# Kernel optimization log

Measured on AMD Instinct MI355X. Metric: run time of the kernel, lower is better.

The kernel has to match this reference:

```python
import jax, jax.numpy as jnp
import numpy as np
import math

HEAD_NUM = 16


def setup_inputs() -> dict:
    key = jax.random.key(0)
    ks = jax.random.split(key, 6)
    B, S, E = 2, 2048, 1024
    sc = 1.0 / math.sqrt(E)
    return {
        "x": jax.random.normal(ks[0], (B, S, E), dtype=jnp.float32),
        "mask": jnp.ones((B, S), dtype=jnp.int32),
        "Wq": jax.random.normal(ks[1], (E, E), dtype=jnp.float32) * sc,
        "bq": jnp.zeros((E,), dtype=jnp.float32),
        "Wk": jax.random.normal(ks[2], (E, E), dtype=jnp.float32) * sc,
        "bk": jnp.zeros((E,), dtype=jnp.float32),
        "Wv": jax.random.normal(ks[3], (E, E), dtype=jnp.float32) * sc,
        "bv": jnp.zeros((E,), dtype=jnp.float32),
        "Wo": jax.random.normal(ks[4], (E, E), dtype=jnp.float32) * sc,
        "bo": jnp.zeros((E,), dtype=jnp.float32),
    }


def reference(x, mask, Wq, bq, Wk, bk, Wv, bv, Wo, bo):
    B, S, E = x.shape
    H = HEAD_NUM
    D = E // H
    # Projections (nn.Linear: x @ W^T + b; W here stored so that x @ W is equivalent)
    q = (x @ Wq + bq).reshape(B, S, H, D).transpose(0, 2, 1, 3)  # [B,H,S,D]
    k = (x @ Wk + bk).reshape(B, S, H, D).transpose(0, 2, 1, 3)
    v = (x @ Wv + bv).reshape(B, S, H, D).transpose(0, 2, 1, 3)
    score = jnp.einsum("bhqd,bhkd->bhqk", q, k) / jnp.sqrt(jnp.asarray(D, x.dtype))
    # Faithful to source: masked positions (mask==0) are filled with +inf
    m = mask[:, None, None, :]  # [B,1,1,S]
    score = jnp.where(m == 0, jnp.inf, score)
    attn = jax.nn.softmax(score, axis=-1)
    # dropout is identity in eval mode
    out = jnp.einsum("bhqk,bhkd->bhqd", attn, v)
    out = out.transpose(0, 2, 1, 3).reshape(B, S, E)
    return out @ Wo + bo
```

## Files before the change

### kernel.cpp

```cpp
#include <hip/hip_runtime.h>
#include <hip/hip_bf16.h>
#include <math.h>


#define S_LEN 2048
#define EMB   1024
#define HN    16
#define HD    64
#define BATCH 2
#define MROWS (BATCH * S_LEN)
#define NEL   ((size_t)MROWS * EMB)

typedef _Float16 f16x8 __attribute__((ext_vector_type(8)));
typedef _Float16 f16x4 __attribute__((ext_vector_type(4)));
typedef _Float16 f16x2 __attribute__((ext_vector_type(2)));
typedef float    f32x4  __attribute__((ext_vector_type(4)));
typedef float    f32x16 __attribute__((ext_vector_type(16)));
typedef unsigned u32x4  __attribute__((ext_vector_type(4)));

#define GLOAD_LDS16(g, l) \
  __builtin_amdgcn_global_load_lds((const __attribute__((address_space(1))) void*)(g), \
                                   (__attribute__((address_space(3))) void*)(l), 16, 0, 0)

__device__ __forceinline__ float exp2fast(float x) {
#if __has_builtin(__builtin_amdgcn_exp2f)
  return __builtin_amdgcn_exp2f(x);
#else
  return __expf(x * 0.69314718056f);
#endif
}

__device__ __forceinline__ unsigned pk_f16(float a, float b) {
#if __has_builtin(__builtin_amdgcn_cvt_pkrtz)
  auto h = __builtin_amdgcn_cvt_pkrtz(a, b);
  return __builtin_bit_cast(unsigned, h);
#else
  unsigned lo = (unsigned)__builtin_bit_cast(unsigned short, (_Float16)a);
  unsigned hi = (unsigned)__builtin_bit_cast(unsigned short, (_Float16)b);
  return lo | (hi << 16);
#endif
}

__device__ __forceinline__ float dot2acc(unsigned p, float acc) {
#if __has_builtin(__builtin_amdgcn_fdot2)
  f16x2 ones = {(_Float16)1.0f, (_Float16)1.0f};
  return __builtin_amdgcn_fdot2(__builtin_bit_cast(f16x2, p), ones, acc, false);
#else
  f16x2 v = __builtin_bit_cast(f16x2, p);
  return acc + (float)v[0] + (float)v[1];
#endif
}

__device__ __forceinline__ f32x16 mfma32(f16x8 a, f16x8 b, f32x16 c) {
  return __builtin_amdgcn_mfma_f32_32x32x16_f16(a, b, c, 0, 0, 0);
}
__device__ __forceinline__ f32x4 mfma16(f16x8 a, f16x8 b, f32x4 c) {
  return __builtin_amdgcn_mfma_f32_16x16x32_f16(a, b, c, 0, 0, 0);
}

__global__ __launch_bounds__(256)
void prep_f16(const float* __restrict__ x,
              const float* __restrict__ Wq, const float* __restrict__ Wk,
              const float* __restrict__ Wv, const float* __restrict__ Wo,
              _Float16* __restrict__ xf, _Float16* __restrict__ Wt,
              _Float16* __restrict__ Wot) {
  __shared__ float tile[64][65];
  const int bid = blockIdx.x;
  const int tt  = threadIdx.x;
  if (bid < 2048) {
    const int i = bid * 256 + tt;
    const float4* s = (const float4*)x + (size_t)i * 2;
    float4 a = s[0], b = s[1];
    f16x8 o = {(_Float16)a.x, (_Float16)a.y, (_Float16)a.z, (_Float16)a.w,
               (_Float16)b.x, (_Float16)b.y, (_Float16)b.z, (_Float16)b.w};
    *((f16x8*)xf + i) = o;
    return;
  }
  const int j   = bid - 2048;
  const int job = j >> 8;
  const int tl  = j & 255;
  const int bn  = (tl & 15) * 64, bk = (tl >> 4) * 64;
  const float* W = (job == 0) ? Wq : (job == 1) ? Wk : (job == 2) ? Wv : Wo;
  _Float16* dst = (job == 3) ? Wot : Wt + (size_t)job * EMB * EMB;
  const int c = tt & 63, r4 = tt >> 6;
#pragma unroll
  for (int jj = 0; jj < 16; ++jj) {
    int r = r4 * 16 + jj;
    tile[r][c] = W[(size_t)(bk + r) * EMB + bn + c];
  }
  __syncthreads();
#pragma unroll
  for (int jj = 0; jj < 16; ++jj) {
    int rr = r4 * 16 + jj;
    dst[(size_t)(bn + rr) * EMB + bk + c] = (_Float16)tile[c][rr];
  }
}

template<bool SW>
__device__ __forceinline__ void gemm_kloop(
    const _Float16* __restrict__ gA, const _Float16* __restrict__ gB,
    _Float16* As, _Float16* Bs, int w,
    int wr, int wc, int ln, int kg, f32x4 (&acc)[4][4]) {
  const int dst = w * 1024;
#define GSTAGE(buf, k0) do { \
    GLOAD_LDS16(gA + (k0),            As + (buf) * 4096 + dst); \
    GLOAD_LDS16(gA + (k0) + 16 * EMB, As + (buf) * 4096 + dst + 512); \
    GLOAD_LDS16(gB + (k0),            Bs + (buf) * 4096 + dst); \
    GLOAD_LDS16(gB + (k0) + 16 * EMB, Bs + (buf) * 4096 + dst + 512); \
  } while (0)
  GSTAGE(0, 0);
  int cur = 0;
#pragma unroll 1
  for (int k0 = 0; k0 < EMB; k0 += 32) {
    __syncthreads();
    if (k0 + 32 < EMB) GSTAGE(cur ^ 1, k0 + 32);
    const _Float16* Ab = As + cur * 4096;
    const _Float16* Bb = Bs + cur * 4096;
    f16x8 a[4], b[4];
#pragma unroll
    for (int mi = 0; mi < 4; ++mi)
      a[mi] = *(const f16x8*)&Ab[(wr * 64 + mi * 16 + ln) * 32 + kg * 8];
#pragma unroll
    for (int ni = 0; ni < 4; ++ni)
      b[ni] = *(const f16x8*)&Bb[(wc * 64 + ni * 16 + ln) * 32 + kg * 8];
#pragma unroll
    for (int mi = 0; mi < 4; ++mi)
#pragma unroll
      for (int ni = 0; ni < 4; ++ni)
        acc[mi][ni] = SW ? mfma16(b[ni], a[mi], acc[mi][ni])
                         : mfma16(a[mi], b[ni], acc[mi][ni]);
    cur ^= 1;
  }
#undef GSTAGE
}

template<int MODE>
__global__ __launch_bounds__(256)
void gemm_f16(const _Float16* __restrict__ A, const _Float16* __restrict__ Bt,
              int Ncols,
              _Float16* __restrict__ qf, _Float16* __restrict__ kf,
              _Float16* __restrict__ vf, float* __restrict__ outF,
              const float* __restrict__ b0, const float* __restrict__ b1,
              const float* __restrict__ b2) {
  __shared__ _Float16 As[2 * 128 * 32];
  __shared__ _Float16 Bs[2 * 128 * 32];
  const int tid  = threadIdx.x;
  const int lane = tid & 63, w = tid >> 6;
  const int ln = lane & 15, kg = lane >> 4;
  const int wr = w >> 1, wc = w & 1;

  const int nbx  = Ncols >> 7;
  const int ncpx = nbx >> 3;
  const int xcd  = blockIdx.x & 7;
  const int idx  = blockIdx.x >> 3;
  const int col0 = (xcd * ncpx + idx % ncpx) << 7;
  const int row0 = (idx / ncpx) << 7;

  const int cA0 = w * 128 + lane;
  const int arow0 = cA0 >> 2, acol0 = (cA0 & 3) * 8;

  f32x4 acc[4][4];
#pragma unroll
  for (int mi = 0; mi < 4; ++mi)
#pragma unroll
    for (int ni = 0; ni < 4; ++ni) acc[mi][ni] = (f32x4){0.f, 0.f, 0.f, 0.f};

  const _Float16* gA = A  + (size_t)(row0 + arow0) * EMB + acol0;
  const _Float16* gB = Bt + (size_t)(col0 + arow0) * EMB + acol0;

  const bool is_v = (MODE == 0) && (col0 >= 2048);
  if (is_v) gemm_kloop<true >(gA, gB, As, Bs, w, wr, wc, ln, kg, acc);
  else      gemm_kloop<false>(gA, gB, As, Bs, w, wr, wc, ln, kg, acc);

  if (MODE == 1) {
#pragma unroll
    for (int mi = 0; mi < 4; ++mi)
#pragma unroll
      for (int ni = 0; ni < 4; ++ni) {
        const int n = col0 + wc * 64 + ni * 16 + ln;
        const float bias = b0[n];
#pragma unroll
        for (int r = 0; r < 4; ++r) {
          const int m = row0 + wr * 64 + mi * 16 + kg * 4 + r;
          outF[(size_t)m * EMB + n] = acc[mi][ni][r] + bias;
        }
      }
  } else if (!is_v) {
#pragma unroll
    for (int mi = 0; mi < 4; ++mi)
#pragma unroll
      for (int ni = 0; ni < 4; ++ni) {
        const int n = col0 + wc * 64 + ni * 16 + ln;
        const int mat = n >> 10, e = n & 1023;
        const float bias = (mat == 0 ? b0 : b1)[e];
        const int h = e >> 6, d = e & 63;
#pragma unroll
        for (int r = 0; r < 4; ++r) {
          const int m = row0 + wr * 64 + mi * 16 + kg * 4 + r;
          const int bb = m >> 11, ss = m & 2047;
          const int bh = bb * HN + h;
          float val = acc[mi][ni][r] + bias;
          if (mat == 0) {
            qf[((size_t)bh * S_LEN + ss) * HD + d] = (_Float16)(val * 0.18033688f);
          } else {
            kf[((size_t)bh * S_LEN + ss) * HD + d] = (_Float16)val;
          }
        }
      }
  } else {
#pragma unroll
    for (int mi = 0; mi < 4; ++mi)
#pragma unroll
      for (int ni = 0; ni < 4; ++ni) {
#pragma unroll
        for (int r = 0; r < 4; ++r) {
          const int n = col0 + wc * 64 + ni * 16 + kg * 4 + r;
          const int e = n - 2048;
          const int h = e >> 6, d = e & 63;
          const int m = row0 + wr * 64 + mi * 16 + ln;
          const int bb = m >> 11, ss = m & 2047;
          const int ssp = (ss & ~12) | ((ss & 4) << 1) | ((ss & 8) >> 1);
          const int bh = bb * HN + h;
          float val = acc[mi][ni][r] + b2[e];
          vf[((size_t)bh * HD + d) * S_LEN + ssp] = (_Float16)val;
        }
      }
  }
}

__global__ __launch_bounds__(512)
void attn_f16v5(const _Float16* __restrict__ Qf, const _Float16* __restrict__ Kf,
                const _Float16* __restrict__ VfT, _Float16* __restrict__ Of) {
  __shared__ _Float16 SH[2][4][4096];

  const int tid  = threadIdx.x;
  const int lane = tid & 63, w = tid >> 6;
  const int ws4  = w & 3, ks = w >> 2;
  const int ql = lane & 31;
  const int hi = lane >> 5;

  const int logical = ((blockIdx.x & 7) << 6) | (blockIdx.x >> 3);
  const int bh = logical >> 4;
  const int qc = logical & 15;
  const int q0w = (qc << 7) + (ws4 << 5);
  const int kbase = ks << 10;

  const size_t qbase = ((size_t)bh * S_LEN + q0w + ql) * HD + hi * 8;
  f16x8 qa[4];
#pragma unroll
  for (int ds = 0; ds < 4; ++ds) qa[ds] = *(const f16x8*)&Qf[qbase + ds * 16];

  f32x16 o0 = {}, o1 = {};
  float lsum = 0.f;

  const int cA = (ws4 << 6) + lane, cB = cA + 256;
  const int rA = cA >> 3, sA = ((cA & 7) ^ (rA & 7)) * 8;
  const int rB = cB >> 3, sB = ((cB & 7) ^ (rB & 7)) * 8;
  const _Float16* KB = Kf  + (size_t)bh * S_LEN * HD;
  const _Float16* VB = VfT + (size_t)bh * HD * S_LEN;

#pragma unroll 1
  for (int t = 0; t < 8; ++t) {
    const int k0 = kbase + t * 128;
    __syncthreads();
    GLOAD_LDS16(KB + (size_t)(k0 + rA) * HD + sA,       &SH[ks][0][cA * 8]);
    GLOAD_LDS16(KB + (size_t)(k0 + rB) * HD + sB,       &SH[ks][0][cB * 8]);
    GLOAD_LDS16(KB + (size_t)(k0 + 64 + rA) * HD + sA,  &SH[ks][1][cA * 8]);
    GLOAD_LDS16(KB + (size_t)(k0 + 64 + rB) * HD + sB,  &SH[ks][1][cB * 8]);
    GLOAD_LDS16(VB + (size_t)rA * S_LEN + k0 + sA,      &SH[ks][2][cA * 8]);
    GLOAD_LDS16(VB + (size_t)rB * S_LEN + k0 + sB,      &SH[ks][2][cB * 8]);
    GLOAD_LDS16(VB + (size_t)rA * S_LEN + k0 + 64 + sA, &SH[ks][3][cA * 8]);
    GLOAD_LDS16(VB + (size_t)rB * S_LEN + k0 + 64 + sB, &SH[ks][3][cB * 8]);
    __syncthreads();

#pragma unroll
    for (int kh = 0; kh < 2; ++kh) {
      const _Float16* Kt = &SH[ks][kh][0];
      const _Float16* Vt = &SH[ks][2 + kh][0];
      f32x16 sf0 = {}, sf1 = {};
#pragma unroll
      for (int ds = 0; ds < 4; ++ds) {
        const int sl = ((ds * 2 + hi) ^ (ql & 7)) * 8;
        f16x8 ka0 = *(const f16x8*)&Kt[ql * 64 + sl];
        f16x8 ka1 = *(const f16x8*)&Kt[(32 + ql) * 64 + sl];
        sf0 = mfma32(ka0, qa[ds], sf0);
        sf1 = mfma32(ka1, qa[ds], sf1);
      }

      unsigned wv[16];
#pragma unroll
      for (int i = 0; i < 8; ++i) {
        float p0 = exp2fast(sf0[2 * i]), p1 = exp2fast(sf0[2 * i + 1]);
        float p2 = exp2fast(sf1[2 * i]), p3 = exp2fast(sf1[2 * i + 1]);
        wv[i]     = pk_f16(p0, p1);
        wv[8 + i] = pk_f16(p2, p3);
        lsum = dot2acc(wv[i], lsum);
        lsum = dot2acc(wv[8 + i], lsum);
      }

#pragma unroll
      for (int kq = 0; kq < 4; ++kq) {
        u32x4 pw = {wv[4 * kq], wv[4 * kq + 1], wv[4 * kq + 2], wv[4 * kq + 3]};
        f16x8 pb = __builtin_bit_cast(f16x8, pw);
        const int sl = ((kq * 2 + hi) ^ (ql & 7)) * 8;
        f16x8 va0 = *(const f16x8*)&Vt[ql * 64 + sl];
        f16x8 va1 = *(const f16x8*)&Vt[(32 + ql) * 64 + sl];
        o0 = mfma32(va0, pb, o0);
        o1 = mfma32(va1, pb, o1);
      }
    }
  }

  __syncthreads();
  float* CMB = reinterpret_cast<float*>(&SH[0][0][0]);
  float* slot = CMB + ((size_t)((ws4 << 6) + lane)) * 36;
  if (ks == 1) {
#pragma unroll
    for (int t = 0; t < 4; ++t) {
      *(f32x4*)&slot[4 * t] =
          (f32x4){o0[4 * t], o0[4 * t + 1], o0[4 * t + 2], o0[4 * t + 3]};
      *(f32x4*)&slot[16 + 4 * t] =
          (f32x4){o1[4 * t], o1[4 * t + 1], o1[4 * t + 2], o1[4 * t + 3]};
    }
    slot[32] = lsum;
  }
  __syncthreads();
  if (ks == 0) {
#pragma unroll
    for (int t = 0; t < 4; ++t) {
      f32x4 a0 = *(const f32x4*)&slot[4 * t];
      f32x4 a1 = *(const f32x4*)&slot[16 + 4 * t];
#pragma unroll
      for (int j = 0; j < 4; ++j) { o0[4 * t + j] += a0[j]; o1[4 * t + j] += a1[j]; }
    }
    lsum += slot[32];
    float lt  = lsum + __shfl_xor(lsum, 32);
    float inv = 1.0f / lt;
    const int b = bh >> 4, h = bh & 15;
    _Float16* ob = Of + ((size_t)(b * S_LEN + q0w + ql)) * EMB + (h << 6);
#pragma unroll
    for (int t = 0; t < 4; ++t) {
      f16x4 v0, v1;
#pragma unroll
      for (int j = 0; j < 4; ++j) {
        v0[j] = (_Float16)(o0[4 * t + j] * inv);
        v1[j] = (_Float16)(o1[4 * t + j] * inv);
      }
      *(f16x4*)&ob[8 * t + 4 * hi]      = v0;
      *(f16x4*)&ob[32 + 8 * t + 4 * hi] = v1;
    }
  }
}


extern "C" void kernel_launch(void* const* d_in, const int* in_sizes, int n_in,
                              void* d_out, int out_size, void* d_ws, size_t ws_size,
                              hipStream_t stream) {
  const float* x  = (const float*)d_in[0];
  const float* Wq = (const float*)d_in[2];
  const float* bq = (const float*)d_in[3];
  const float* Wk = (const float*)d_in[4];
  const float* bk = (const float*)d_in[5];
  const float* Wv = (const float*)d_in[6];
  const float* bv = (const float*)d_in[7];
  const float* Wo = (const float*)d_in[8];
  const float* bo = (const float*)d_in[9];
  float* out = (float*)d_out;

  _Float16* Qf  = (_Float16*)d_ws;
  _Float16* Kf  = Qf + NEL;
  _Float16* VfT = Kf + NEL;
  _Float16* xf  = VfT + NEL;
  _Float16* Of  = xf;
  _Float16* Wt  = xf + NEL;
  _Float16* Wot = Wt + 3 * (size_t)EMB * EMB;

  prep_f16<<<dim3(3072), 256, 0, stream>>>(x, Wq, Wk, Wv, Wo, xf, Wt, Wot);

  gemm_f16<0><<<dim3((MROWS / 128) * (3072 / 128)), 256, 0, stream>>>(
      xf, Wt, 3072, Qf, Kf, VfT, nullptr, bq, bk, bv);

  attn_f16v5<<<dim3(BATCH * HN * (S_LEN / 128)), 512, 0, stream>>>(
      Qf, Kf, VfT, Of);

  gemm_f16<1><<<dim3((MROWS / 128) * (EMB / 128)), 256, 0, stream>>>(
      Of, Wot, 1024, nullptr, nullptr, nullptr, out, bo, nullptr, nullptr);
}
```

Measured before the change: 124.4 us.

## Switch projection GEMMs to 32x32 MFMA with BK=64 and XOR-swizzled LDS

Reworks the shared GEMM k-loop to use 32x32x16 MFMA tiles (2x2 per wave) in place of 16x16x32 tiles (4x4 per wave). The k-step grows from 32 to 64, halving the number of barriers and loop iterations. Global-to-LDS loads now use an XOR swizzle on the 16-byte chunk index to avoid LDS bank conflicts on the wider rows. This doubles LDS use per block, and the epilogues are remapped to the 32x32 accumulator layout, which adds risk of indexing errors and of lower occupancy.

```diff
diff --git a/kernel.cpp b/kernel.cpp
--- a/kernel.cpp
+++ b/kernel.cpp
@@ -53,9 +53,6 @@
 
 __device__ __forceinline__ f32x16 mfma32(f16x8 a, f16x8 b, f32x16 c) {
   return __builtin_amdgcn_mfma_f32_32x32x16_f16(a, b, c, 0, 0, 0);
-}
-__device__ __forceinline__ f32x4 mfma16(f16x8 a, f16x8 b, f32x4 c) {
-  return __builtin_amdgcn_mfma_f32_16x16x32_f16(a, b, c, 0, 0, 0);
 }
 
 __global__ __launch_bounds__(256)
@@ -99,36 +96,44 @@
 template<bool SW>
 __device__ __forceinline__ void gemm_kloop(
     const _Float16* __restrict__ gA, const _Float16* __restrict__ gB,
-    _Float16* As, _Float16* Bs, int w,
-    int wr, int wc, int ln, int kg, f32x4 (&acc)[4][4]) {
-  const int dst = w * 1024;
+    _Float16* As, _Float16* Bs, int tid, int wr, int wc, int ql, int hi,
+    f32x16 (&acc)[2][2]) {
 #define GSTAGE(buf, k0) do { \
-    GLOAD_LDS16(gA + (k0),            As + (buf) * 4096 + dst); \
-    GLOAD_LDS16(gA + (k0) + 16 * EMB, As + (buf) * 4096 + dst + 512); \
-    GLOAD_LDS16(gB + (k0),            Bs + (buf) * 4096 + dst); \
-    GLOAD_LDS16(gB + (k0) + 16 * EMB, Bs + (buf) * 4096 + dst + 512); \
+    _Pragma("unroll") \
+    for (int j = 0; j < 4; ++j) { \
+      const int c = tid + j * 256; \
+      const int row = c >> 3, sl = ((c & 7) ^ (row & 7)) * 8; \
+      GLOAD_LDS16(gA + (size_t)row * EMB + (k0) + sl, As + (buf) * 8192 + c * 8); \
+      GLOAD_LDS16(gB + (size_t)row * EMB + (k0) + sl, Bs + (buf) * 8192 + c * 8); \
+    } \
   } while (0)
   GSTAGE(0, 0);
   int cur = 0;
 #pragma unroll 1
-  for (int k0 = 0; k0 < EMB; k0 += 32) {
+  for (int k0 = 0; k0 < EMB; k0 += 64) {
     __syncthreads();
-    if (k0 + 32 < EMB) GSTAGE(cur ^ 1, k0 + 32);
-    const _Float16* Ab = As + cur * 4096;
-    const _Float16* Bb = Bs + cur * 4096;
-    f16x8 a[4], b[4];
-#pragma unroll
-    for (int mi = 0; mi < 4; ++mi)
-      a[mi] = *(const f16x8*)&Ab[(wr * 64 + mi * 16 + ln) * 32 + kg * 8];
-#pragma unroll
-    for (int ni = 0; ni < 4; ++ni)
-      b[ni] = *(const f16x8*)&Bb[(wc * 64 + ni * 16 + ln) * 32 + kg * 8];
-#pragma unroll
-    for (int mi = 0; mi < 4; ++mi)
-#pragma unroll
-      for (int ni = 0; ni < 4; ++ni)
-        acc[mi][ni] = SW ? mfma16(b[ni], a[mi], acc[mi][ni])
-                         : mfma16(a[mi], b[ni], acc[mi][ni]);
+    if (k0 + 64 < EMB) GSTAGE(cur ^ 1, k0 + 64);
+    const _Float16* Ab = As + cur * 8192;
+    const _Float16* Bb = Bs + cur * 8192;
+#pragma unroll
+    for (int ks = 0; ks < 4; ++ks) {
+      const int sl = (((ks << 1) | hi) ^ (ql & 7)) << 3;
+      f16x8 a0 = *(const f16x8*)&Ab[(wr * 64 + ql) * 64 + sl];
+      f16x8 a1 = *(const f16x8*)&Ab[(wr * 64 + 32 + ql) * 64 + sl];
+      f16x8 b0 = *(const f16x8*)&Bb[(wc * 64 + ql) * 64 + sl];
+      f16x8 b1 = *(const f16x8*)&Bb[(wc * 64 + 32 + ql) * 64 + sl];
+      if (SW) {
+        acc[0][0] = mfma32(b0, a0, acc[0][0]);
+        acc[0][1] = mfma32(b1, a0, acc[0][1]);
+        acc[1][0] = mfma32(b0, a1, acc[1][0]);
+        acc[1][1] = mfma32(b1, a1, acc[1][1]);
+      } else {
+        acc[0][0] = mfma32(a0, b0, acc[0][0]);
+        acc[0][1] = mfma32(a0, b1, acc[0][1]);
+        acc[1][0] = mfma32(a1, b0, acc[1][0]);
+        acc[1][1] = mfma32(a1, b1, acc[1][1]);
+      }
+    }
     cur ^= 1;
   }
 #undef GSTAGE
@@ -142,11 +147,11 @@
               _Float16* __restrict__ vf, float* __restrict__ outF,
               const float* __restrict__ b0, const float* __restrict__ b1,
               const float* __restrict__ b2) {
-  __shared__ _Float16 As[2 * 128 * 32];
-  __shared__ _Float16 Bs[2 * 128 * 32];
+  __shared__ _Float16 As[2 * 128 * 64];
+  __shared__ _Float16 Bs[2 * 128 * 64];
   const int tid  = threadIdx.x;
   const int lane = tid & 63, w = tid >> 6;
-  const int ln = lane & 15, kg = lane >> 4;
+  const int ql = lane & 31, hi = lane >> 5;
   const int wr = w >> 1, wc = w & 1;
 
   const int nbx  = Ncols >> 7;
@@ -156,47 +161,44 @@
   const int col0 = (xcd * ncpx + idx % ncpx) << 7;
   const int row0 = (idx / ncpx) << 7;
 
-  const int cA0 = w * 128 + lane;
-  const int arow0 = cA0 >> 2, acol0 = (cA0 & 3) * 8;
-
-  f32x4 acc[4][4];
-#pragma unroll
-  for (int mi = 0; mi < 4; ++mi)
-#pragma unroll
-    for (int ni = 0; ni < 4; ++ni) acc[mi][ni] = (f32x4){0.f, 0.f, 0.f, 0.f};
-
-  const _Float16* gA = A  + (size_t)(row0 + arow0) * EMB + acol0;
-  const _Float16* gB = Bt + (size_t)(col0 + arow0) * EMB + acol0;
+  f32x16 acc[2][2];
+#pragma unroll
+  for (int mi = 0; mi < 2; ++mi)
+#pragma unroll
+    for (int ni = 0; ni < 2; ++ni) acc[mi][ni] = (f32x16){};
+
+  const _Float16* gA = A  + (size_t)row0 * EMB;
+  const _Float16* gB = Bt + (size_t)col0 * EMB;
 
   const bool is_v = (MODE == 0) && (col0 >= 2048);
-  if (is_v) gemm_kloop<true >(gA, gB, As, Bs, w, wr, wc, ln, kg, acc);
-  else      gemm_kloop<false>(gA, gB, As, Bs, w, wr, wc, ln, kg, acc);
+  if (is_v) gemm_kloop<true >(gA, gB, As, Bs, tid, wr, wc, ql, hi, acc);
+  else      gemm_kloop<false>(gA, gB, As, Bs, tid, wr, wc, ql, hi, acc);
 
   if (MODE == 1) {
 #pragma unroll
-    for (int mi = 0; mi < 4; ++mi)
-#pragma unroll
-      for (int ni = 0; ni < 4; ++ni) {
-        const int n = col0 + wc * 64 + ni * 16 + ln;
+    for (int mi = 0; mi < 2; ++mi)
+#pragma unroll
+      for (int ni = 0; ni < 2; ++ni) {
+        const int n = col0 + wc * 64 + ni * 32 + ql;
         const float bias = b0[n];
 #pragma unroll
-        for (int r = 0; r < 4; ++r) {
-          const int m = row0 + wr * 64 + mi * 16 + kg * 4 + r;
+        for (int r = 0; r < 16; ++r) {
+          const int m = row0 + wr * 64 + mi * 32 + (r & 3) + 8 * (r >> 2) + 4 * hi;
           outF[(size_t)m * EMB + n] = acc[mi][ni][r] + bias;
         }
       }
   } else if (!is_v) {
 #pragma unroll
-    for (int mi = 0; mi < 4; ++mi)
-#pragma unroll
-      for (int ni = 0; ni < 4; ++ni) {
-        const int n = col0 + wc * 64 + ni * 16 + ln;
+    for (int mi = 0; mi < 2; ++mi)
+#pragma unroll
+      for (int ni = 0; ni < 2; ++ni) {
+        const int n = col0 + wc * 64 + ni * 32 + ql;
         const int mat = n >> 10, e = n & 1023;
         const float bias = (mat == 0 ? b0 : b1)[e];
         const int h = e >> 6, d = e & 63;
 #pragma unroll
-        for (int r = 0; r < 4; ++r) {
-          const int m = row0 + wr * 64 + mi * 16 + kg * 4 + r;
+        for (int r = 0; r < 16; ++r) {
+          const int m = row0 + wr * 64 + mi * 32 + (r & 3) + 8 * (r >> 2) + 4 * hi;
           const int bb = m >> 11, ss = m & 2047;
           const int bh = bb * HN + h;
           float val = acc[mi][ni][r] + bias;
@@ -209,22 +211,23 @@
       }
   } else {
 #pragma unroll
-    for (int mi = 0; mi < 4; ++mi)
-#pragma unroll
-      for (int ni = 0; ni < 4; ++ni) {
-#pragma unroll
-        for (int r = 0; r < 4; ++r) {
-          const int n = col0 + wc * 64 + ni * 16 + kg * 4 + r;
+    for (int mi = 0; mi < 2; ++mi) {
+      const int m = row0 + wr * 64 + mi * 32 + ql;
+      const int bb = m >> 11, ss = m & 2047;
+      const int ssp = (ss & ~12) | ((ss & 4) << 1) | ((ss & 8) >> 1);
+#pragma unroll
+      for (int ni = 0; ni < 2; ++ni) {
+#pragma unroll
+        for (int r = 0; r < 16; ++r) {
+          const int n = col0 + wc * 64 + ni * 32 + (r & 3) + 8 * (r >> 2) + 4 * hi;
           const int e = n - 2048;
           const int h = e >> 6, d = e & 63;
-          const int m = row0 + wr * 64 + mi * 16 + ln;
-          const int bb = m >> 11, ss = m & 2047;
-          const int ssp = (ss & ~12) | ((ss & 4) << 1) | ((ss & 8) >> 1);
           const int bh = bb * HN + h;
           float val = acc[mi][ni][r] + b2[e];
           vf[((size_t)bh * HD + d) * S_LEN + ssp] = (_Float16)val;
         }
       }
+    }
   }
 }
 
```

New measurement: 117.6 us. 5.5% less time.
